# Performance work log

Measured on AMD Instinct MI355X. Metric: run time of the kernel, lower is better.

Reference implementation:

```python
import jax, jax.numpy as jnp
import numpy as np

B, C, T = 128, 272, 1024
D1, K = 270, 32


def setup_inputs() -> dict:
    key = jax.random.key(0)
    k1, k2, k3, k4 = jax.random.split(key, 4)
    X = jax.random.normal(k1, (B, C, T), dtype=jnp.float32)
    loc = jax.random.uniform(k2, (C, 2), dtype=jnp.float32)  # 2D sensor coords in [0,1]
    z_re = jax.random.normal(k3, (D1, K, K), dtype=jnp.float32)
    z_im = jax.random.normal(k4, (D1, K, K), dtype=jnp.float32)
    return {"X": X, "loc": loc, "z_re": z_re, "z_im": z_im}


def reference(X, loc, z_re, z_im):
    # X: [B, C, T]; loc: [C, 2]; z_re/z_im: [D1, K, K]
    Kdim = z_re.shape[1]
    x, y = loc[:, 0], loc[:, 1]                      # [C]
    k = jnp.arange(Kdim, dtype=X.dtype)
    # phase[k, l, c] = 2*pi*(k*x[c] + l*y[c])
    phase = 2.0 * jnp.pi * (k[:, None, None] * x[None, None, :]
                            + k[None, :, None] * y[None, None, :])  # [K, K, C]
    # a[j, c] = sum_{k,l} z_re[j,k,l]*cos(phase) + z_im[j,k,l]*sin(phase)
    A = (jnp.einsum('dkl,klc->dc', z_re, jnp.cos(phase))
         + jnp.einsum('dkl,klc->dc', z_im, jnp.sin(phase)))  # [D1, C]
    # exp(a_j) / sum_c exp(a_j) == softmax over channels (same math)
    w = jax.nn.softmax(A, axis=1)                    # [D1, C]
    # out[b, j, t] = sum_c w[j,c] * X[b,c,t]
    return jnp.einsum('dc,bct->bdt', w, X)           # [B, D1, T]
```

## Files before the change

### kernel.cpp

```cpp
#include <hip/hip_runtime.h>

#define BB 128
#define CC 272
#define TT 1024
#define DD 270
#define KK 32
#define NKC 9
#define NMT 17
#define MP 272
#define WBYTES (NKC * NMT * 64 * 16)

typedef __attribute__((ext_vector_type(8))) short s16x8;
typedef __attribute__((ext_vector_type(4))) float f32x4;

__device__ __forceinline__ unsigned short f2bf(float f) {
  unsigned int u = __builtin_bit_cast(unsigned int, f);
  u += 0x7fffu + ((u >> 16) & 1u);
  return (unsigned short)(u >> 16);
}

__global__ __launch_bounds__(288) void phaseA_kernel(
    const float* __restrict__ loc, const float* __restrict__ z_re,
    const float* __restrict__ z_im, float* __restrict__ A) {
  const int d = blockIdx.x;
  const int p = blockIdx.y;
  const int c = threadIdx.x;
  if (c >= CC) return;
  const float TWO_PI = 6.28318530717958647692f;
  float x = loc[2 * c], y = loc[2 * c + 1];
  float sx, cx, sy, cyv;
  sincosf(TWO_PI * x, &sx, &cx);
  sincosf(TWO_PI * y, &sy, &cyv);
  float cl[KK], sl[KK];
  cl[0] = 1.f; sl[0] = 0.f;
#pragma unroll
  for (int l = 1; l < KK; ++l) {
    cl[l] = cl[l - 1] * cyv - sl[l - 1] * sy;
    sl[l] = sl[l - 1] * cyv + cl[l - 1] * sy;
  }
  const int k0 = p * 8;
  float sk, ck;
  sincosf(TWO_PI * (float)k0 * x, &sk, &ck);
  const float* zr = z_re + (size_t)d * (KK * KK) + k0 * KK;
  const float* zi = z_im + (size_t)d * (KK * KK) + k0 * KK;
  float acc = 0.f;
  for (int k = 0; k < 8; ++k) {
    float s_rc = 0.f, s_rs = 0.f, s_ic = 0.f, s_is = 0.f;
#pragma unroll
    for (int l = 0; l < KK; ++l) {
      float vr = zr[k * KK + l];
      float vi = zi[k * KK + l];
      s_rc += vr * cl[l];
      s_rs += vr * sl[l];
      s_ic += vi * cl[l];
      s_is += vi * sl[l];
    }
    acc += ck * (s_rc + s_is) + sk * (s_ic - s_rs);
    float nck = ck * cx - sk * sx;
    sk = sk * cx + ck * sx;
    ck = nck;
  }
  atomicAdd(&A[d * CC + c], acc);
}

__global__ __launch_bounds__(64) void softmax_kernel(
    const float* __restrict__ A, unsigned short* __restrict__ wb) {
  const int d = blockIdx.x;
  const int lane = threadIdx.x;
  const bool live = (d < DD);
  float v[5];
  float inv = 0.f;
  if (live) {
    float m = -3.0e38f;
#pragma unroll
    for (int j = 0; j < 5; ++j) {
      int cidx = lane + 64 * j;
      v[j] = (cidx < CC) ? A[(size_t)d * CC + cidx] : -3.0e38f;
      m = fmaxf(m, v[j]);
    }
#pragma unroll
    for (int off = 32; off >= 1; off >>= 1) m = fmaxf(m, __shfl_xor(m, off, 64));
    float s = 0.f;
#pragma unroll
    for (int j = 0; j < 5; ++j) {
      int cidx = lane + 64 * j;
      v[j] = (cidx < CC) ? expf(v[j] - m) : 0.f;
      s += v[j];
    }
#pragma unroll
    for (int off = 32; off >= 1; off >>= 1) s += __shfl_xor(s, off, 64);
    inv = 1.f / s;
  }
  const int mt = d >> 4, mrow = d & 15;
#pragma unroll
  for (int j = 0; j < 5; ++j) {
    int kk = lane + 64 * j;
    if (kk < NKC * KK) {
      unsigned short val = 0;
      if (live && kk < CC) val = f2bf(v[j] * inv);
      int kc = kk >> 5, hi = (kk >> 3) & 3, jj = kk & 7;
      wb[((size_t)(kc * NMT + mt) << 9) + (((hi << 4) | mrow) << 3) + jj] = val;
    }
  }
}

__global__ __launch_bounds__(256, 2) void gemm_kernel(
    const float* __restrict__ X, const unsigned short* __restrict__ wb,
    float* __restrict__ out) {
  const int bid = blockIdx.x;
  const int b = bid >> 4;
  const int t0 = (bid & 15) << 6;
  const int tid = threadIdx.x;
  const int lane = tid & 63;
  const int dw = tid >> 6;
  const int q = lane >> 4;
  const int r16 = lane & 15;
  const bool has5 = (dw == 0);

  f32x4 acc[5][4];
#pragma unroll
  for (int i = 0; i < 5; ++i)
#pragma unroll
    for (int f = 0; f < 4; ++f) acc[i][f] = (f32x4){0.f, 0.f, 0.f, 0.f};

  const unsigned short* wf = wb + (size_t)lane * 8;
  const float* Xb = X + (size_t)b * (CC * TT) + t0 + r16;
  const int csub = q << 3;

  s16x8 a_cur[5], a_nxt[5];
  float xf[32], xn[32];

#pragma unroll
  for (int i = 0; i < 4; ++i)
    a_cur[i] = *(const s16x8*)(wf + ((size_t)(dw + (i << 2)) << 9));
  if (has5) a_cur[4] = *(const s16x8*)(wf + ((size_t)16 << 9));
#pragma unroll
  for (int f = 0; f < 4; ++f)
#pragma unroll
    for (int j = 0; j < 8; ++j)
      xf[f * 8 + j] = Xb[(size_t)(csub + j) * TT + (f << 4)];

#pragma unroll
  for (int kc = 0; kc < NKC; ++kc) {
    if (kc < NKC - 1) {
      const int cb = (kc + 1) * KK + csub;
#pragma unroll
      for (int i = 0; i < 4; ++i)
        a_nxt[i] = *(const s16x8*)(wf + ((size_t)((kc + 1) * NMT + dw + (i << 2)) << 9));
      if (has5)
        a_nxt[4] = *(const s16x8*)(wf + ((size_t)((kc + 1) * NMT + 16) << 9));
#pragma unroll
      for (int f = 0; f < 4; ++f)
#pragma unroll
        for (int j = 0; j < 8; ++j)
          xn[f * 8 + j] = (cb + j < CC) ? Xb[(size_t)(cb + j) * TT + (f << 4)] : 0.f;
    }
    union { unsigned int u[4]; s16x8 v; } bf[4];
#pragma unroll
    for (int f = 0; f < 4; ++f)
#pragma unroll
      for (int p = 0; p < 4; ++p)
        bf[f].u[p] = (unsigned int)f2bf(xf[f * 8 + 2 * p]) |
                     ((unsigned int)f2bf(xf[f * 8 + 2 * p + 1]) << 16);
#pragma unroll
    for (int i = 0; i < 4; ++i)
#pragma unroll
      for (int f = 0; f < 4; ++f)
        acc[i][f] = __builtin_amdgcn_mfma_f32_16x16x32_bf16(a_cur[i], bf[f].v, acc[i][f], 0, 0, 0);
    if (has5) {
#pragma unroll
      for (int f = 0; f < 4; ++f)
        acc[4][f] = __builtin_amdgcn_mfma_f32_16x16x32_bf16(a_cur[4], bf[f].v, acc[4][f], 0, 0, 0);
    }
#pragma unroll
    for (int i = 0; i < 5; ++i) a_cur[i] = a_nxt[i];
#pragma unroll
    for (int v2 = 0; v2 < 32; ++v2) xf[v2] = xn[v2];
  }

  float* op = out + (size_t)b * (DD * TT) + t0 + r16;
#pragma unroll
  for (int i = 0; i < 4; ++i) {
    const int mtb = (dw + (i << 2)) << 4;
#pragma unroll
    for (int f = 0; f < 4; ++f)
#pragma unroll
      for (int r = 0; r < 4; ++r)
        op[(size_t)(mtb + q * 4 + r) * TT + (f << 4)] = acc[i][f][r];
  }
  if (has5) {
#pragma unroll
    for (int f = 0; f < 4; ++f)
#pragma unroll
      for (int r = 0; r < 4; ++r) {
        const int drow = 256 + q * 4 + r;
        if (drow < DD) op[(size_t)drow * TT + (f << 4)] = acc[4][f][r];
      }
  }
}

extern "C" void kernel_launch(void* const* d_in, const int* in_sizes, int n_in,
                              void* d_out, int out_size, void* d_ws, size_t ws_size,
                              hipStream_t stream) {
  const float* X = (const float*)d_in[0];
  const float* loc = (const float*)d_in[1];
  const float* z_re = (const float*)d_in[2];
  const float* z_im = (const float*)d_in[3];
  float* out = (float*)d_out;

  float* A = (float*)d_ws;
  unsigned short* wbf = (unsigned short*)((char*)d_ws + 294912);

  hipMemsetAsync(A, 0, DD * CC * sizeof(float), stream);
  phaseA_kernel<<<dim3(DD, 4), 288, 0, stream>>>(loc, z_re, z_im, A);
  softmax_kernel<<<MP, 64, 0, stream>>>(A, wbf);
  gemm_kernel<<<BB * (TT / 64), 256, 0, stream>>>(X, wbf, out);
}
```

Measured before the change: 325.2 us.

## Stage X tiles through LDS with async global_load_lds in a 4-deep pipeline

The GEMM kernel no longer has each wave load X straight from global memory into registers. X chunks are staged into a four-buffer LDS ring with global_load_lds, issued three chunks ahead, using an XOR-swizzled layout, and read back from LDS after barriers. All four waves now compute the fifth M tile redundantly rather than only wave 0, which removes the divergence at the cost of extra MFMAs. The code also adds hand-placed vmcnt/lgkmcnt waits and two barriers per iteration, and it depends on exact counts of outstanding memory operations.

```diff
diff --git a/kernel.cpp b/kernel.cpp
--- a/kernel.cpp
+++ b/kernel.cpp
@@ -8,7 +8,6 @@
 #define NKC 9
 #define NMT 17
 #define MP 272
-#define WBYTES (NKC * NMT * 64 * 16)
 
 typedef __attribute__((ext_vector_type(8))) short s16x8;
 typedef __attribute__((ext_vector_type(4))) float f32x4;
@@ -107,6 +106,7 @@
 __global__ __launch_bounds__(256, 2) void gemm_kernel(
     const float* __restrict__ X, const unsigned short* __restrict__ wb,
     float* __restrict__ out) {
+  __shared__ float xs[4][KK * 64];
   const int bid = blockIdx.x;
   const int b = bid >> 4;
   const int t0 = (bid & 15) << 6;
@@ -115,7 +115,35 @@
   const int dw = tid >> 6;
   const int q = lane >> 4;
   const int r16 = lane & 15;
-  const bool has5 = (dw == 0);
+
+  const unsigned short* wf = wb + (size_t)lane * 8;
+  const float* Xb = X + (size_t)b * (CC * TT) + t0;
+
+  int scl[2], stf[2];
+#pragma unroll
+  for (int r = 0; r < 2; ++r) {
+    int idx = tid + (r << 8);
+    scl[r] = idx >> 4;
+    stf[r] = ((idx & 15) << 2) ^ (((idx >> 7) & 3) << 4);
+  }
+
+#define STAGE(KC_, BUF_) do {                                              \
+    const int kcs_ = (KC_);                                                \
+    float* dstb_ = &xs[(BUF_)][0];                                         \
+    _Pragma("unroll")                                                      \
+    for (int r_ = 0; r_ < 2; ++r_) {                                       \
+      int idx_ = tid + (r_ << 8);                                          \
+      int cg_ = kcs_ * KK + scl[r_];                                       \
+      if (cg_ > CC - 1) cg_ = CC - 1;       \
+      const float* src_ = Xb + (size_t)cg_ * TT + stf[r_];                 \
+      __builtin_amdgcn_global_load_lds(                                    \
+          (const __attribute__((address_space(1))) unsigned int*)src_,     \
+          (__attribute__((address_space(3))) unsigned int*)(dstb_ + idx_ * 4), \
+          16, 0, 0);                                                       \
+    }                                                                      \
+  } while (0)
+
+  int mti[5] = {dw, dw + 4, dw + 8, dw + 12, 16};
 
   f32x4 acc[5][4];
 #pragma unroll
@@ -123,60 +151,69 @@
 #pragma unroll
     for (int f = 0; f < 4; ++f) acc[i][f] = (f32x4){0.f, 0.f, 0.f, 0.f};
 
-  const unsigned short* wf = wb + (size_t)lane * 8;
-  const float* Xb = X + (size_t)b * (CC * TT) + t0 + r16;
-  const int csub = q << 3;
+  int tq[4];
+#pragma unroll
+  for (int f = 0; f < 4; ++f) tq[f] = ((f << 4) + r16) ^ (q << 4);
+  const int crow = q << 3;
 
   s16x8 a_cur[5], a_nxt[5];
-  float xf[32], xn[32];
-
-#pragma unroll
-  for (int i = 0; i < 4; ++i)
-    a_cur[i] = *(const s16x8*)(wf + ((size_t)(dw + (i << 2)) << 9));
-  if (has5) a_cur[4] = *(const s16x8*)(wf + ((size_t)16 << 9));
-#pragma unroll
-  for (int f = 0; f < 4; ++f)
-#pragma unroll
-    for (int j = 0; j < 8; ++j)
-      xf[f * 8 + j] = Xb[(size_t)(csub + j) * TT + (f << 4)];
+
+  STAGE(0, 0);
+  asm volatile("" ::: "memory");
+  STAGE(1, 1);
+  STAGE(2, 2);
+#pragma unroll
+  for (int i = 0; i < 5; ++i)
+    a_cur[i] = *(const s16x8*)(wf + ((size_t)mti[i] << 9));
 
 #pragma unroll
   for (int kc = 0; kc < NKC; ++kc) {
-    if (kc < NKC - 1) {
-      const int cb = (kc + 1) * KK + csub;
-#pragma unroll
-      for (int i = 0; i < 4; ++i)
-        a_nxt[i] = *(const s16x8*)(wf + ((size_t)((kc + 1) * NMT + dw + (i << 2)) << 9));
-      if (has5)
-        a_nxt[4] = *(const s16x8*)(wf + ((size_t)((kc + 1) * NMT + 16) << 9));
+    {
+      const int kcs = (kc + 3 < NKC) ? kc + 3 : NKC - 1;
+      STAGE(kcs, (kc + 3) & 3);
+    }
+    if (kc == 0) {
+      asm volatile("s_waitcnt vmcnt(11)" ::: "memory");
+    }
+    __builtin_amdgcn_s_barrier();
+    asm volatile("" ::: "memory");
+
+    float tmp[32];
+    {
+      const float* bufp = &xs[kc & 3][0];
 #pragma unroll
       for (int f = 0; f < 4; ++f)
 #pragma unroll
         for (int j = 0; j < 8; ++j)
-          xn[f * 8 + j] = (cb + j < CC) ? Xb[(size_t)(cb + j) * TT + (f << 4)] : 0.f;
-    }
+          tmp[f * 8 + j] = bufp[(crow + j) * 64 + tq[f]];
+    }
+    asm volatile("s_waitcnt lgkmcnt(0)" ::: "memory");
+    __builtin_amdgcn_s_barrier();
+
+    {
+      const int kca = (kc + 1 < NKC) ? kc + 1 : NKC - 1;
+#pragma unroll
+      for (int i = 0; i < 5; ++i)
+        a_nxt[i] = *(const s16x8*)(wf + ((size_t)(kca * NMT + mti[i]) << 9));
+    }
+    asm volatile("s_waitcnt vmcnt(7)" ::: "memory");
+
     union { unsigned int u[4]; s16x8 v; } bf[4];
 #pragma unroll
     for (int f = 0; f < 4; ++f)
 #pragma unroll
       for (int p = 0; p < 4; ++p)
-        bf[f].u[p] = (unsigned int)f2bf(xf[f * 8 + 2 * p]) |
-                     ((unsigned int)f2bf(xf[f * 8 + 2 * p + 1]) << 16);
-#pragma unroll
-    for (int i = 0; i < 4; ++i)
+        bf[f].u[p] = (unsigned int)f2bf(tmp[f * 8 + 2 * p]) |
+                     ((unsigned int)f2bf(tmp[f * 8 + 2 * p + 1]) << 16);
+#pragma unroll
+    for (int i = 0; i < 5; ++i)
 #pragma unroll
       for (int f = 0; f < 4; ++f)
         acc[i][f] = __builtin_amdgcn_mfma_f32_16x16x32_bf16(a_cur[i], bf[f].v, acc[i][f], 0, 0, 0);
-    if (has5) {
-#pragma unroll
-      for (int f = 0; f < 4; ++f)
-        acc[4][f] = __builtin_amdgcn_mfma_f32_16x16x32_bf16(a_cur[4], bf[f].v, acc[4][f], 0, 0, 0);
-    }
 #pragma unroll
     for (int i = 0; i < 5; ++i) a_cur[i] = a_nxt[i];
-#pragma unroll
-    for (int v2 = 0; v2 < 32; ++v2) xf[v2] = xn[v2];
-  }
+  }
+#undef STAGE
 
   float* op = out + (size_t)b * (DD * TT) + t0 + r16;
 #pragma unroll
@@ -188,7 +225,7 @@
       for (int r = 0; r < 4; ++r)
         op[(size_t)(mtb + q * 4 + r) * TT + (f << 4)] = acc[i][f][r];
   }
-  if (has5) {
+  if (dw == 0) {
 #pragma unroll
     for (int f = 0; f < 4; ++f)
 #pragma unroll
```

Measured after the change: 318.5 us. 2.1% less time.

## Halve GEMM time tile and deepen X prefetch to three stages

Applied to the files above, without the earlier changes.

The GEMM block now covers 32 time steps instead of 64, which doubles the grid and halves the accumulator and X register footprint per thread. X loads use a triple-buffered register pipeline that prefetches three K-chunks ahead. The 17th M-tile is now computed by every warp instead of only warp 0, removing divergence. The catch is that warps 1-3 do redundant MFMA work on that tile, and each block reuses the weight fragments over fewer columns.

```diff
diff --git a/kernel.cpp b/kernel.cpp
--- a/kernel.cpp
+++ b/kernel.cpp
@@ -8,7 +8,6 @@
 #define NKC 9
 #define NMT 17
 #define MP 272
-#define WBYTES (NKC * NMT * 64 * 16)
 
 typedef __attribute__((ext_vector_type(8))) short s16x8;
 typedef __attribute__((ext_vector_type(4))) float f32x4;
@@ -108,89 +107,91 @@
     const float* __restrict__ X, const unsigned short* __restrict__ wb,
     float* __restrict__ out) {
   const int bid = blockIdx.x;
-  const int b = bid >> 4;
-  const int t0 = (bid & 15) << 6;
+  const int b = bid >> 5;
+  const int t0 = (bid & 31) << 5;
   const int tid = threadIdx.x;
   const int lane = tid & 63;
   const int dw = tid >> 6;
   const int q = lane >> 4;
   const int r16 = lane & 15;
-  const bool has5 = (dw == 0);
-
-  f32x4 acc[5][4];
+  const int csub = q << 3;
+
+  const unsigned short* wfl = wb + (size_t)lane * 8;
+  const float* Xb = X + (size_t)b * (CC * TT) + t0 + r16;
+
+  f32x4 acc[5][2];
 #pragma unroll
   for (int i = 0; i < 5; ++i)
 #pragma unroll
-    for (int f = 0; f < 4; ++f) acc[i][f] = (f32x4){0.f, 0.f, 0.f, 0.f};
-
-  const unsigned short* wf = wb + (size_t)lane * 8;
-  const float* Xb = X + (size_t)b * (CC * TT) + t0 + r16;
-  const int csub = q << 3;
-
-  s16x8 a_cur[5], a_nxt[5];
-  float xf[32], xn[32];
-
-#pragma unroll
-  for (int i = 0; i < 4; ++i)
-    a_cur[i] = *(const s16x8*)(wf + ((size_t)(dw + (i << 2)) << 9));
-  if (has5) a_cur[4] = *(const s16x8*)(wf + ((size_t)16 << 9));
-#pragma unroll
-  for (int f = 0; f < 4; ++f)
-#pragma unroll
-    for (int j = 0; j < 8; ++j)
-      xf[f * 8 + j] = Xb[(size_t)(csub + j) * TT + (f << 4)];
-
-#pragma unroll
-  for (int kc = 0; kc < NKC; ++kc) {
-    if (kc < NKC - 1) {
-      const int cb = (kc + 1) * KK + csub;
-#pragma unroll
-      for (int i = 0; i < 4; ++i)
-        a_nxt[i] = *(const s16x8*)(wf + ((size_t)((kc + 1) * NMT + dw + (i << 2)) << 9));
-      if (has5)
-        a_nxt[4] = *(const s16x8*)(wf + ((size_t)((kc + 1) * NMT + 16) << 9));
-#pragma unroll
-      for (int f = 0; f < 4; ++f)
-#pragma unroll
-        for (int j = 0; j < 8; ++j)
-          xn[f * 8 + j] = (cb + j < CC) ? Xb[(size_t)(cb + j) * TT + (f << 4)] : 0.f;
-    }
-    union { unsigned int u[4]; s16x8 v; } bf[4];
-#pragma unroll
-    for (int f = 0; f < 4; ++f)
-#pragma unroll
-      for (int p = 0; p < 4; ++p)
-        bf[f].u[p] = (unsigned int)f2bf(xf[f * 8 + 2 * p]) |
-                     ((unsigned int)f2bf(xf[f * 8 + 2 * p + 1]) << 16);
-#pragma unroll
-    for (int i = 0; i < 4; ++i)
-#pragma unroll
-      for (int f = 0; f < 4; ++f)
-        acc[i][f] = __builtin_amdgcn_mfma_f32_16x16x32_bf16(a_cur[i], bf[f].v, acc[i][f], 0, 0, 0);
-    if (has5) {
-#pragma unroll
-      for (int f = 0; f < 4; ++f)
-        acc[4][f] = __builtin_amdgcn_mfma_f32_16x16x32_bf16(a_cur[4], bf[f].v, acc[4][f], 0, 0, 0);
-    }
-#pragma unroll
-    for (int i = 0; i < 5; ++i) a_cur[i] = a_nxt[i];
-#pragma unroll
-    for (int v2 = 0; v2 < 32; ++v2) xf[v2] = xn[v2];
-  }
+    for (int f = 0; f < 2; ++f) acc[i][f] = (f32x4){0.f, 0.f, 0.f, 0.f};
+
+#define MTI(I) ((I) < 4 ? dw + 4 * (I) : 16)
+#define ALOAD(KC, I) (*(const s16x8*)(wfl + ((size_t)((KC) * NMT + MTI(I)) << 9)))
+#define XLOAD(DST, KC)                                                  \
+  {                                                                     \
+    _Pragma("unroll") for (int j = 0; j < 8; ++j) {                     \
+      int c_ = (KC) * KK + csub + j;                                    \
+      float v0_ = 0.f, v1_ = 0.f;                                       \
+      if ((KC) < 8 || c_ < CC) {                                        \
+        v0_ = Xb[(size_t)c_ * TT];                                      \
+        v1_ = Xb[(size_t)c_ * TT + 16];                                 \
+      }                                                                 \
+      DST[j] = v0_;                                                     \
+      DST[8 + j] = v1_;                                                 \
+    }                                                                   \
+  }
+
+  s16x8 ac[5], an[5];
+  float x0[16], x1[16], x2[16];
+
+  XLOAD(x0, 0);
+  XLOAD(x1, 1);
+  XLOAD(x2, 2);
+#pragma unroll
+  for (int i = 0; i < 5; ++i) ac[i] = ALOAD(0, i);
+
+#define BODY(KC, XC)                                                          \
+  {                                                                           \
+    if ((KC) + 1 < NKC) {                                                     \
+      _Pragma("unroll") for (int i = 0; i < 5; ++i) an[i] = ALOAD((KC) + 1, i); \
+    }                                                                         \
+    union { unsigned int u[4]; s16x8 v; } bf[2];                              \
+    _Pragma("unroll") for (int f = 0; f < 2; ++f)                             \
+        _Pragma("unroll") for (int p = 0; p < 4; ++p)                         \
+        bf[f].u[p] = (unsigned int)f2bf(XC[f * 8 + 2 * p]) |                  \
+                     ((unsigned int)f2bf(XC[f * 8 + 2 * p + 1]) << 16);       \
+    if ((KC) + 3 < NKC) { XLOAD(XC, (KC) + 3); }                              \
+    _Pragma("unroll") for (int i = 0; i < 5; ++i)                             \
+        _Pragma("unroll") for (int f = 0; f < 2; ++f)                         \
+        acc[i][f] = __builtin_amdgcn_mfma_f32_16x16x32_bf16(ac[i], bf[f].v,   \
+                                                            acc[i][f], 0, 0, 0); \
+    if ((KC) + 1 < NKC) {                                                     \
+      _Pragma("unroll") for (int i = 0; i < 5; ++i) ac[i] = an[i];            \
+    }                                                                         \
+  }
+
+  BODY(0, x0) BODY(1, x1) BODY(2, x2)
+  BODY(3, x0) BODY(4, x1) BODY(5, x2)
+  BODY(6, x0) BODY(7, x1) BODY(8, x2)
+
+#undef BODY
+#undef XLOAD
+#undef ALOAD
+#undef MTI
 
   float* op = out + (size_t)b * (DD * TT) + t0 + r16;
 #pragma unroll
   for (int i = 0; i < 4; ++i) {
     const int mtb = (dw + (i << 2)) << 4;
 #pragma unroll
-    for (int f = 0; f < 4; ++f)
+    for (int f = 0; f < 2; ++f)
 #pragma unroll
       for (int r = 0; r < 4; ++r)
         op[(size_t)(mtb + q * 4 + r) * TT + (f << 4)] = acc[i][f][r];
   }
-  if (has5) {
-#pragma unroll
-    for (int f = 0; f < 4; ++f)
+  if (dw == 0) {
+#pragma unroll
+    for (int f = 0; f < 2; ++f)
 #pragma unroll
       for (int r = 0; r < 4; ++r) {
         const int drow = 256 + q * 4 + r;
@@ -214,5 +215,5 @@
   hipMemsetAsync(A, 0, DD * CC * sizeof(float), stream);
   phaseA_kernel<<<dim3(DD, 4), 288, 0, stream>>>(loc, z_re, z_im, A);
   softmax_kernel<<<MP, 64, 0, stream>>>(A, wbf);
-  gemm_kernel<<<BB * (TT / 64), 256, 0, stream>>>(X, wbf, out);
-}
+  gemm_kernel<<<BB * (TT / 32), 256, 0, stream>>>(X, wbf, out);
+}
```

Result: slower. 356.4 us (+9.6%).
